# Kernel optimization log

Hardware: AMD Instinct MI355X
Metric: run time of the kernel (lower is better)

Reference implementation:

```python
import jax, jax.numpy as jnp
from jax import lax
import numpy as np

N = 10000      # num_nodes
T = 24         # hist_len
IN_DIM = 16
HID = 128
HEADS = 4
E = 160000     # num_edges
PRED = 24
NEG_SLOPE = 0.2  # GATv2 LeakyReLU default


def _lstm_layer(xs, wih, whh, bih, bhh):
    # xs: [T, N, D]; PyTorch gate order i, f, g, o
    Hh = whh.shape[1]
    h0 = jnp.zeros((xs.shape[1], Hh), xs.dtype)
    def step(carry, xt):
        h, c = carry
        g = xt @ wih.T + bih + h @ whh.T + bhh
        i, f, gg, o = jnp.split(g, 4, axis=-1)
        c = jax.nn.sigmoid(f) * c + jax.nn.sigmoid(i) * jnp.tanh(gg)
        h = jax.nn.sigmoid(o) * jnp.tanh(c)
        return (h, c), h
    (_, _), out = lax.scan(step, (h0, h0), xs)
    return out  # [T, N, Hh]


def _gatv2(z, src, dst, wl, bl, wr, br, att, bias):
    # PyG GATv2Conv: share_weights=False, concat=True, add_self_loops=False
    n = z.shape[0]
    xl = (z @ wl.T + bl).reshape(n, HEADS, HID)   # source/message transform
    xr = (z @ wr.T + br).reshape(n, HEADS, HID)   # target transform
    e = jax.nn.leaky_relu(xl[src] + xr[dst], NEG_SLOPE)   # [E, H, C]
    score = jnp.einsum('ehc,hc->eh', e, att)              # [E, H]
    smax = jax.ops.segment_max(score, dst, num_segments=n)
    p = jnp.exp(score - smax[dst])
    denom = jax.ops.segment_sum(p, dst, num_segments=n)
    alpha = p / (denom[dst] + 1e-16)                      # segment softmax over in-edges
    out = jax.ops.segment_sum(xl[src] * alpha[:, :, None], dst, num_segments=n)
    return out.reshape(n, HEADS * HID) + bias


def setup_inputs() -> dict:
    key = jax.random.key(0)
    ks = iter(jax.random.split(key, 64))
    def W(shape):
        return jax.random.normal(next(ks), shape, jnp.float32) / np.sqrt(shape[-1])
    inp = {}
    inp['x'] = jax.random.normal(next(ks), (N, T, IN_DIM), jnp.float32)
    inp['edge_index'] = jax.random.randint(next(ks), (2, E), 0, N, jnp.int32)
    inp['mlp_in_w0'] = W((HID, IN_DIM)); inp['mlp_in_b0'] = jnp.zeros((HID,), jnp.float32)
    inp['mlp_in_w1'] = W((HID, HID));    inp['mlp_in_b1'] = jnp.zeros((HID,), jnp.float32)
    for l in range(2):  # nn.LSTM(num_layers = lstm_num_layers*2 = 2)
        inp[f'lstm_wih{l}'] = W((4 * HID, HID))
        inp[f'lstm_whh{l}'] = W((4 * HID, HID))
        inp[f'lstm_bih{l}'] = jnp.zeros((4 * HID,), jnp.float32)
        inp[f'lstm_bhh{l}'] = jnp.zeros((4 * HID,), jnp.float32)
    for l in range(2):  # nGAT_layer = 2
        inp[f'gat{l}_wl'] = W((HEADS * HID, HID))
        inp[f'gat{l}_bl'] = jnp.zeros((HEADS * HID,), jnp.float32)
        inp[f'gat{l}_wr'] = W((HEADS * HID, HID))
        inp[f'gat{l}_br'] = jnp.zeros((HEADS * HID,), jnp.float32)
        inp[f'gat{l}_att'] = W((HEADS, HID))
        inp[f'gat{l}_bias'] = jnp.zeros((HEADS * HID,), jnp.float32)
        inp[f'gat{l}_pw'] = W((HID, HEADS * HID))
        inp[f'gat{l}_pb'] = jnp.zeros((HID,), jnp.float32)
    inp['mlp_out_w0'] = W((HID, HID));  inp['mlp_out_b0'] = jnp.zeros((HID,), jnp.float32)
    inp['mlp_out_w1'] = W((PRED, HID)); inp['mlp_out_b1'] = jnp.zeros((PRED,), jnp.float32)
    return inp


def _forward(x, edge_index, mlp_in_w0, mlp_in_b0, mlp_in_w1, mlp_in_b1,
             lstm_wih0, lstm_whh0, lstm_bih0, lstm_bhh0,
             lstm_wih1, lstm_whh1, lstm_bih1, lstm_bhh1,
             gat0_wl, gat0_bl, gat0_wr, gat0_br, gat0_att, gat0_bias, gat0_pw, gat0_pb,
             gat1_wl, gat1_bl, gat1_wr, gat1_br, gat1_att, gat1_bias, gat1_pw, gat1_pb,
             mlp_out_w0, mlp_out_b0, mlp_out_w1, mlp_out_b1):
    src, dst = edge_index[0], edge_index[1]
    h = jnp.transpose(x, (1, 0, 2))                       # [T, N, in_dim]
    # MLP_layers_in: Linear(in,hid), Linear(hid,hid), ReLU
    h = h @ mlp_in_w0.T + mlp_in_b0
    h = jax.nn.relu(h @ mlp_in_w1.T + mlp_in_b1)
    # 2-layer unidirectional LSTM
    h = _lstm_layer(h, lstm_wih0, lstm_whh0, lstm_bih0, lstm_bhh0)
    h = _lstm_layer(h, lstm_wih1, lstm_whh1, lstm_bih1, lstm_bhh1)
    z = h[-1]                                             # [N, HID] last timestep
    # GAT block x2: GATv2Conv -> Linear(heads*hid, hid) -> ReLU
    z = _gatv2(z, src, dst, gat0_wl, gat0_bl, gat0_wr, gat0_br, gat0_att, gat0_bias)
    z = jax.nn.relu(z @ gat0_pw.T + gat0_pb)
    z = _gatv2(z, src, dst, gat1_wl, gat1_bl, gat1_wr, gat1_br, gat1_att, gat1_bias)
    z = jax.nn.relu(z @ gat1_pw.T + gat1_pb)
    # MLP_layers_out: Linear(hid,hid), ReLU, Linear(hid, pred_len)
    z = jax.nn.relu(z @ mlp_out_w0.T + mlp_out_b0)
    return z @ mlp_out_w1.T + mlp_out_b1                  # [N, PRED]


def reference(x, edge_index, mlp_in_w0, mlp_in_b0, mlp_in_w1, mlp_in_b1,
              lstm_wih0, lstm_whh0, lstm_bih0, lstm_bhh0,
              lstm_wih1, lstm_whh1, lstm_bih1, lstm_bhh1,
              gat0_wl, gat0_bl, gat0_wr, gat0_br, gat0_att, gat0_bias, gat0_pw, gat0_pb,
              gat1_wl, gat1_bl, gat1_wr, gat1_br, gat1_att, gat1_bias, gat1_pw, gat1_pb,
              mlp_out_w0, mlp_out_b0, mlp_out_w1, mlp_out_b1):
    return _forward(x, edge_index, mlp_in_w0, mlp_in_b0, mlp_in_w1, mlp_in_b1,
                    lstm_wih0, lstm_whh0, lstm_bih0, lstm_bhh0,
                    lstm_wih1, lstm_whh1, lstm_bih1, lstm_bhh1,
                    gat0_wl, gat0_bl, gat0_wr, gat0_br, gat0_att, gat0_bias, gat0_pw, gat0_pb,
                    gat1_wl, gat1_bl, gat1_wr, gat1_br, gat1_att, gat1_bias, gat1_pw, gat1_pb,
                    mlp_out_w0, mlp_out_b0, mlp_out_w1, mlp_out_b1)
```

## Files before the change

kernel.cpp:

```cpp
#include <hip/hip_runtime.h>
#include <hip/hip_bf16.h>

#define NNODES 10000
#define TLEN 24
#define INDIM 16
#define HID 128
#define GDIM 512

typedef __hip_bfloat16 bf16;
typedef short v8s __attribute__((ext_vector_type(8)));
typedef float v4f __attribute__((ext_vector_type(4)));

__device__ inline float u2f(unsigned u){ return __uint_as_float(u); }

__device__ inline void unpack8(uint4 v, float* f){
  f[0]=u2f(v.x<<16); f[1]=u2f(v.x&0xFFFF0000u);
  f[2]=u2f(v.y<<16); f[3]=u2f(v.y&0xFFFF0000u);
  f[4]=u2f(v.z<<16); f[5]=u2f(v.z&0xFFFF0000u);
  f[6]=u2f(v.w<<16); f[7]=u2f(v.w&0xFFFF0000u);
}

__device__ inline float fsig(float x){
  return __builtin_amdgcn_rcpf(1.f + __expf(-x));
}
__device__ inline float ftanh(float x){
  float t = __expf(-2.f*fabsf(x));
  float r = (1.f - t) * __builtin_amdgcn_rcpf(1.f + t);
  return copysignf(r, x);
}

__global__ __launch_bounds__(256) void conv_w_k(
    const float* s0, const float* s1, const float* s2, const float* s3,
    const float* s4, const float* s5, const float* s6, const float* s7,
    const float* s8, const float* s9, const float* s10,
    bf16* __restrict__ dst, int* __restrict__ deg)
{
  int idx = blockIdx.x*256 + threadIdx.x;
  if (idx < NNODES) deg[idx] = 0;
  if (idx >= 671744) return;
  int c = idx >> 16;
  float v;
  if (c < 10){
    const float* srcs[10] = {s0,s1,s2,s3,s4,s5,s6,s7,s8,s9};
    v = srcs[c][idx & 0xFFFF];
  } else {
    v = s10[idx - 655360];
  }
  dst[idx] = __float2bfloat16(v);
}

__global__ void prep_w_k(
    const float* __restrict__ miw0, const float* __restrict__ mib0,
    const float* __restrict__ miw1, const float* __restrict__ mib1,
    const float* __restrict__ bih0, const float* __restrict__ bhh0,
    const float* __restrict__ bih1, const float* __restrict__ bhh1,
    const float* __restrict__ bl0, const float* __restrict__ br0,
    const float* __restrict__ bl1, const float* __restrict__ br1,
    float* __restrict__ Wp, float* __restrict__ bp,
    float* __restrict__ bsum, float* __restrict__ gblr)
{
  int t = threadIdx.x;
  for (int idx = t; idx < HID*INDIM; idx += 256){
    int j = idx >> 4, d = idx & 15;
    float s = 0.f;
    for (int k=0;k<HID;k++) s += miw1[j*HID+k] * miw0[k*INDIM+d];
    Wp[idx] = s;
  }
  for (int j = t; j < HID; j += 256){
    float s = mib1[j];
    for (int k=0;k<HID;k++) s += miw1[j*HID+k] * mib0[k];
    bp[j] = s;
  }
  for (int i = t; i < GDIM; i += 256){
    bsum[i]        = bih0[i] + bhh0[i];
    bsum[GDIM + i] = bih1[i] + bhh1[i];
  }
  for (int i = t; i < GDIM; i += 256){
    gblr[i]          = bl0[i];
    gblr[GDIM + i]   = br0[i];
    gblr[1024 + i]   = bl1[i];
    gblr[1536 + i]   = br1[i];
  }
}

__global__ __launch_bounds__(256) void mlp_in_k(
    const float* __restrict__ x, const float* __restrict__ Wp,
    const float* __restrict__ bp, bf16* __restrict__ X0)
{
  __shared__ __align__(16) float xs[64*16];
  const int tid = threadIdx.x;
  const int m0 = blockIdx.x*64;
  {
    int row = tid >> 2, q = tid & 3;
    int m = m0 + row;
    int t = m / NNODES, n = m - t*NNODES;
    float4 v = *(const float4*)(x + ((size_t)n*TLEN + t)*INDIM + q*4);
    *(float4*)(xs + row*16 + q*4) = v;
  }
  const int j = tid & 127;
  const int half = tid >> 7;
  const float* wr = Wp + j*INDIM;
  float4 w0 = *(const float4*)(wr);
  float4 w1 = *(const float4*)(wr + 4);
  float4 w2 = *(const float4*)(wr + 8);
  float4 w3 = *(const float4*)(wr + 12);
  float bj = bp[j];
  __syncthreads();
  #pragma unroll 4
  for (int mi=0; mi<32; mi++){
    int row = mi*2 + half;
    const float* xr = xs + row*16;
    float4 a0 = *(const float4*)(xr);
    float4 a1 = *(const float4*)(xr + 4);
    float4 a2 = *(const float4*)(xr + 8);
    float4 a3 = *(const float4*)(xr + 12);
    float s = bj
      + a0.x*w0.x + a0.y*w0.y + a0.z*w0.z + a0.w*w0.w
      + a1.x*w1.x + a1.y*w1.y + a1.z*w1.z + a1.w*w1.w
      + a2.x*w2.x + a2.y*w2.y + a2.z*w2.z + a2.w*w2.w
      + a3.x*w3.x + a3.y*w3.y + a3.z*w3.z + a3.w*w3.w;
    s = s > 0.f ? s : 0.f;
    X0[(size_t)(m0+row)*HID + j] = __float2bfloat16(s);
  }
}

template<int WRITE_ALL>
__global__ __launch_bounds__(512) void lstm_half(
    const bf16* __restrict__ Xin, const bf16* __restrict__ Wih,
    const bf16* __restrict__ Whh, const float* __restrict__ bias,
    bf16* __restrict__ out)
{
  __shared__ __align__(16) bf16 hsA[16*136];
  __shared__ __align__(16) bf16 hsB[16*136];
  const int tid = threadIdx.x;
  const int lane = tid & 63, w = tid >> 6;
  const int r16 = lane & 15, quad = lane >> 4;
  const int m0 = blockIdx.x*16;

  v8s wbi[4][4], wbh[4][4];
  #pragma unroll
  for (int g=0; g<4; g++)
    #pragma unroll
    for (int kc=0; kc<4; kc++){
      size_t o = (size_t)(g*HID + w*16 + r16)*HID + kc*32 + quad*8;
      wbi[g][kc] = *(const v8s*)(Wih + o);
      wbh[g][kc] = *(const v8s*)(Whh + o);
    }
  float bg[4];
  #pragma unroll
  for (int g=0; g<4; g++) bg[g] = bias[g*HID + w*16 + r16];

  const size_t rowoff = (size_t)(m0 + r16) * HID;

  float c[4];
  #pragma unroll
  for (int i=0;i<4;i++) c[i] = 0.f;

  for (int i = tid; i < 272; i += 512){
    *(uint4*)((char*)hsA + i*16) = make_uint4(0,0,0,0);
    *(uint4*)((char*)hsB + i*16) = make_uint4(0,0,0,0);
  }

  v8s ax[4];
  #pragma unroll
  for (int kc=0; kc<4; kc++)
    ax[kc] = *(const v8s*)(Xin + rowoff + kc*32 + quad*8);

  __syncthreads();

  #pragma unroll 1
  for (int t=0; t<TLEN; t++){
    bf16* hrd = (t & 1) ? hsA : hsB;
    bf16* hwr = (t & 1) ? hsB : hsA;

    v4f acc[4];
    #pragma unroll
    for (int g=0;g<4;g++) acc[g] = (v4f)0.f;

    #pragma unroll
    for (int kc=0; kc<4; kc++)
      #pragma unroll
      for (int g=0;g<4;g++)
        acc[g] = __builtin_amdgcn_mfma_f32_16x16x32_bf16(ax[kc], wbi[g][kc], acc[g], 0, 0, 0);

    {
      int tn = t+1 < TLEN ? t+1 : TLEN-1;
      const bf16* Xn = Xin + (size_t)tn*NNODES*HID;
      #pragma unroll
      for (int kc=0; kc<4; kc++)
        ax[kc] = *(const v8s*)(Xn + rowoff + kc*32 + quad*8);
    }

    #pragma unroll
    for (int kc=0; kc<4; kc++){
      v8s av = *(const v8s*)(hrd + r16*136 + kc*32 + quad*8);
      #pragma unroll
      for (int g=0;g<4;g++)
        acc[g] = __builtin_amdgcn_mfma_f32_16x16x32_bf16(av, wbh[g][kc], acc[g], 0, 0, 0);
    }

    #pragma unroll
    for (int r=0;r<4;r++){
      int lrow = quad*4 + r;
      float iv = acc[0][r] + bg[0];
      float fv = acc[1][r] + bg[1];
      float gv = acc[2][r] + bg[2];
      float ov = acc[3][r] + bg[3];
      float ig = fsig(iv), fg = fsig(fv);
      float gg = ftanh(gv), og = fsig(ov);
      float cn = fg*c[r] + ig*gg;
      c[r] = cn;
      hwr[lrow*136 + w*16 + r16] = __float2bfloat16(og*ftanh(cn));
    }
    __syncthreads();

    if (WRITE_ALL){
      bf16* dst = (bf16*)(Xin + (size_t)t*NNODES*HID);
      for (int i = tid; i < 256; i += 512){
        int row = i >> 4, c8 = (i & 15) * 8;
        *(uint4*)(dst + (size_t)(m0+row)*HID + c8) = *(const uint4*)(hwr + row*136 + c8);
      }
    }
  }

  if (!WRITE_ALL){
    const bf16* hfin = ((TLEN-1) & 1) ? hsB : hsA;
    for (int i = tid; i < 256; i += 512){
      int row = i >> 4, c8 = (i & 15) * 8;
      *(uint4*)(out + (size_t)(m0+row)*HID + c8) = *(const uint4*)(hfin + row*136 + c8);
    }
  }
}

template<int ACT>
__global__ __launch_bounds__(256) void gemm_bt(
    const bf16* __restrict__ A, const bf16* __restrict__ B,
    const float* __restrict__ bias, bf16* __restrict__ C,
    int M, int N, int K)
{
  __shared__ __align__(16) bf16 As[128*40];
  __shared__ __align__(16) bf16 Bs[128*40];
  const int tid = threadIdx.x;
  const int m0 = blockIdx.x*128, n0 = blockIdx.y*128;
  const int lane = tid & 63, wave = tid >> 6;
  const int r16 = lane & 15, quad = lane >> 4;

  v4f acc[2][8];
  #pragma unroll
  for (int a=0;a<2;a++)
    #pragma unroll
    for (int b=0;b<8;b++) acc[a][b] = (v4f)0.f;

  for (int k0=0; k0<K; k0+=32){
    #pragma unroll
    for (int i=0;i<2;i++){
      int li = tid + i*256;
      int row = li >> 2, q4 = li & 3;
      uint4 va = make_uint4(0,0,0,0);
      int gm = m0 + row;
      if (gm < M) va = *(const uint4*)(A + (size_t)gm*K + k0 + q4*8);
      *(uint4*)(As + row*40 + q4*8) = va;
      uint4 vb = make_uint4(0,0,0,0);
      int gn = n0 + row;
      if (gn < N) vb = *(const uint4*)(B + (size_t)gn*K + k0 + q4*8);
      *(uint4*)(Bs + row*40 + q4*8) = vb;
    }
    __syncthreads();
    v8s av[2], bv[8];
    #pragma unroll
    for (int mi=0;mi<2;mi++)
      av[mi] = *(const v8s*)(As + (wave*32 + mi*16 + r16)*40 + quad*8);
    #pragma unroll
    for (int ni=0;ni<8;ni++)
      bv[ni] = *(const v8s*)(Bs + (ni*16 + r16)*40 + quad*8);
    #pragma unroll
    for (int mi=0;mi<2;mi++)
      #pragma unroll
      for (int ni=0;ni<8;ni++)
        acc[mi][ni] = __builtin_amdgcn_mfma_f32_16x16x32_bf16(av[mi], bv[ni], acc[mi][ni], 0, 0, 0);
    __syncthreads();
  }

  #pragma unroll
  for (int mi=0;mi<2;mi++){
    #pragma unroll
    for (int r=0;r<4;r++){
      int row = m0 + wave*32 + mi*16 + quad*4 + r;
      if (row >= M) continue;
      #pragma unroll
      for (int ni=0;ni<8;ni++){
        int col = n0 + ni*16 + r16;
        float v = acc[mi][ni][r] + bias[col];
        if (ACT == 1) v = v > 0.f ? v : 0.f;
        C[(size_t)row*N + col] = __float2bfloat16(v);
      }
    }
  }
}

template<int ACT>
__global__ __launch_bounds__(256) void gemm_bt64(
    const bf16* __restrict__ A, const bf16* __restrict__ B,
    const float* __restrict__ bias, bf16* __restrict__ C,
    int M, int K)
{
  __shared__ __align__(16) bf16 As[64*40];
  __shared__ __align__(16) bf16 Bs[128*40];
  const int tid = threadIdx.x;
  const int m0 = blockIdx.x*64;
  const int lane = tid & 63, wave = tid >> 6;
  const int r16 = lane & 15, quad = lane >> 4;

  v4f acc[8];
  #pragma unroll
  for (int b=0;b<8;b++) acc[b] = (v4f)0.f;

  for (int k0=0; k0<K; k0+=32){
    {
      int row = tid >> 2, q4 = tid & 3;
      uint4 va = make_uint4(0,0,0,0);
      int gm = m0 + row;
      if (gm < M) va = *(const uint4*)(A + (size_t)gm*K + k0 + q4*8);
      *(uint4*)(As + row*40 + q4*8) = va;
    }
    #pragma unroll
    for (int i=0;i<2;i++){
      int li = tid + i*256;
      int row = li >> 2, q4 = li & 3;
      uint4 vb = *(const uint4*)(B + (size_t)row*K + k0 + q4*8);
      *(uint4*)(Bs + row*40 + q4*8) = vb;
    }
    __syncthreads();
    v8s av, bv[8];
    av = *(const v8s*)(As + (wave*16 + r16)*40 + quad*8);
    #pragma unroll
    for (int ni=0;ni<8;ni++)
      bv[ni] = *(const v8s*)(Bs + (ni*16 + r16)*40 + quad*8);
    #pragma unroll
    for (int ni=0;ni<8;ni++)
      acc[ni] = __builtin_amdgcn_mfma_f32_16x16x32_bf16(av, bv[ni], acc[ni], 0, 0, 0);
    __syncthreads();
  }

  #pragma unroll
  for (int r=0;r<4;r++){
    int row = m0 + wave*16 + quad*4 + r;
    if (row >= M) continue;
    #pragma unroll
    for (int ni=0;ni<8;ni++){
      int col = ni*16 + r16;
      float v = acc[ni][r] + bias[col];
      if (ACT == 1) v = v > 0.f ? v : 0.f;
      C[(size_t)row*HID + col] = __float2bfloat16(v);
    }
  }
}

__global__ void deg_count_k(const int* __restrict__ dst, int* __restrict__ deg, int E){
  int e = blockIdx.x*256 + threadIdx.x;
  if (e < E){
    unsigned d = (unsigned)dst[e];
    if (d < (unsigned)NNODES) atomicAdd(&deg[d], 1);
  }
}

__global__ void scan_k(const int* __restrict__ deg, int* __restrict__ offs,
                       int* __restrict__ cursor, int n)
{
  __shared__ int part[256];
  __shared__ int base[256];
  int t = threadIdx.x;
  int lo = t*40, hi = lo+40;
  if (lo > n) lo = n;
  if (hi > n) hi = n;
  int s = 0;
  for (int i=lo;i<hi;i++) s += deg[i];
  part[t] = s;
  __syncthreads();
  if (t == 0){
    int run=0;
    for (int i=0;i<256;i++){ base[i]=run; run+=part[i]; }
    offs[n] = run;
  }
  __syncthreads();
  int run = base[t];
  for (int i=lo;i<hi;i++){ offs[i]=run; cursor[i]=run; run += deg[i]; }
}

__global__ void fill_k(const int* __restrict__ src, const int* __restrict__ dst,
                       int* __restrict__ cursor, int* __restrict__ srcs, int E){
  int e = blockIdx.x*256 + threadIdx.x;
  if (e < E){
    unsigned d = (unsigned)dst[e];
    if (d < (unsigned)NNODES){
      int p = atomicAdd(&cursor[d], 1);
      unsigned s = (unsigned)src[e];
      srcs[p] = (s < (unsigned)NNODES) ? (int)s : 0;
    }
  }
}

__global__ __launch_bounds__(256) void gat_onl(
    const int* __restrict__ offs, const int* __restrict__ srcs,
    const bf16* __restrict__ xc, const float* __restrict__ att,
    const float* __restrict__ gbias, bf16* __restrict__ agg)
{
  int d = blockIdx.x*4 + (threadIdx.x >> 6);
  if (d >= NNODES) return;
  int lane = threadIdx.x & 63;
  float fr[8];
  unpack8(*(const uint4*)(xc + (size_t)d*1024 + 512 + lane*8), fr);
  float4 a0 = *(const float4*)(att + lane*8);
  float4 a1 = *(const float4*)(att + lane*8 + 4);
  float fa[8] = {a0.x,a0.y,a0.z,a0.w,a1.x,a1.y,a1.z,a1.w};
  int i0 = offs[d], i1 = offs[d+1];

  float m = -3.4e38f, den = 0.f;
  float acc[8] = {0,0,0,0,0,0,0,0};

  if (i0 < i1){
    uint4 raw = *(const uint4*)(xc + (size_t)srcs[i0]*1024 + lane*8);
    for (int i=i0; i<i1; i++){
      uint4 nxt;
      if (i+1 < i1)
        nxt = *(const uint4*)(xc + (size_t)srcs[i+1]*1024 + lane*8);
      float fl[8];
      unpack8(raw, fl);
      float p = 0.f;
      #pragma unroll
      for (int q=0;q<8;q++){
        float v = fl[q] + fr[q];
        v = v > 0.f ? v : 0.2f*v;
        p += v*fa[q];
      }
      p += __shfl_xor(p, 1); p += __shfl_xor(p, 2);
      p += __shfl_xor(p, 4); p += __shfl_xor(p, 8);
      float mn = fmaxf(m, p);
      float corr = __expf(m - mn);
      float w = __expf(p - mn);
      den = den*corr + w;
      #pragma unroll
      for (int q=0;q<8;q++) acc[q] = acc[q]*corr + w*fl[q];
      m = mn;
      raw = nxt;
    }
  }
  float r = 1.f/(den + 1e-16f);
  float4 b0 = *(const float4*)(gbias + lane*8);
  float4 b1 = *(const float4*)(gbias + lane*8 + 4);
  float fb[8] = {b0.x,b0.y,b0.z,b0.w,b1.x,b1.y,b1.z,b1.w};
  #pragma unroll
  for (int q=0;q<8;q++)
    agg[(size_t)d*GDIM + lane*8 + q] = __float2bfloat16(acc[q]*r + fb[q]);
}

__global__ __launch_bounds__(256) void mlp_final_k(
    const bf16* __restrict__ a, const float* __restrict__ w,
    const float* __restrict__ b, float* __restrict__ out)
{
  int g = blockIdx.x*256 + threadIdx.x;
  if (g >= NNODES*24) return;
  int j = g % 24;
  int row = g / 24;
  const bf16* ar = a + (size_t)row*HID;
  const float* wr = w + (size_t)j*HID;
  float s = b[j];
  for (int k=0;k<HID;k+=8){
    float fa[8];
    unpack8(*(const uint4*)(ar+k), fa);
    float4 w0 = *(const float4*)(wr + k);
    float4 w1 = *(const float4*)(wr + k + 4);
    s += fa[0]*w0.x + fa[1]*w0.y + fa[2]*w0.z + fa[3]*w0.w
       + fa[4]*w1.x + fa[5]*w1.y + fa[6]*w1.z + fa[7]*w1.w;
  }
  out[g] = s;
}


extern "C" void kernel_launch(void* const* d_in, const int* in_sizes, int n_in,
                              void* d_out, int out_size, void* d_ws, size_t ws_size,
                              hipStream_t stream)
{
  const float* x   = (const float*)d_in[0];
  const int*   ei  = (const int*)d_in[1];
  const int E = in_sizes[1] / 2;
  const int* srcp = ei;
  const int* dstp = ei + E;

  const float* miw0 = (const float*)d_in[2];
  const float* mib0 = (const float*)d_in[3];
  const float* miw1 = (const float*)d_in[4];
  const float* mib1 = (const float*)d_in[5];
  const float* wih0 = (const float*)d_in[6];
  const float* whh0 = (const float*)d_in[7];
  const float* bih0 = (const float*)d_in[8];
  const float* bhh0 = (const float*)d_in[9];
  const float* wih1 = (const float*)d_in[10];
  const float* whh1 = (const float*)d_in[11];
  const float* bih1 = (const float*)d_in[12];
  const float* bhh1 = (const float*)d_in[13];
  const float* g_wl[2]   = {(const float*)d_in[14], (const float*)d_in[22]};
  const float* g_bl[2]   = {(const float*)d_in[15], (const float*)d_in[23]};
  const float* g_wr[2]   = {(const float*)d_in[16], (const float*)d_in[24]};
  const float* g_br[2]   = {(const float*)d_in[17], (const float*)d_in[25]};
  const float* g_att[2]  = {(const float*)d_in[18], (const float*)d_in[26]};
  const float* g_bias[2] = {(const float*)d_in[19], (const float*)d_in[27]};
  const float* g_pw[2]   = {(const float*)d_in[20], (const float*)d_in[28]};
  const float* g_pb[2]   = {(const float*)d_in[21], (const float*)d_in[29]};
  const float* mow0 = (const float*)d_in[30];
  const float* mob0 = (const float*)d_in[31];
  const float* mow1 = (const float*)d_in[32];
  const float* mob1 = (const float*)d_in[33];
  (void)n_in; (void)out_size; (void)ws_size;

  char* base = (char*)d_ws;
  size_t off = 0;
  auto carve = [&](size_t n)->char*{
    char* p = base + off;
    off = (off + n + 255) & ~(size_t)255;
    return p;
  };
  char*  X0r = carve((size_t)TLEN*NNODES*HID*2);
  bf16*  zf  = (bf16*)carve((size_t)NNODES*HID*2);
  float* Wp  = (float*)carve(HID*INDIM*4);
  float* bp  = (float*)carve(HID*4);
  float* bsum= (float*)carve(2*GDIM*4);
  float* gblr= (float*)carve(2*1024*4);
  bf16*  wbf = (bf16*)carve((size_t)671744*2);
  int*   offsb = (int*)carve((size_t)(NNODES+1)*4);
  int*   curs  = (int*)carve((size_t)NNODES*4);
  int*   srcs  = (int*)carve((size_t)E*4);
  int*   deg   = (int*)carve((size_t)NNODES*4);
  bf16*  agg   = (bf16*)carve((size_t)NNODES*GDIM*2);

  const bf16* wih0b = wbf + 0;
  const bf16* whh0b = wbf + 65536;
  const bf16* wih1b = wbf + 131072;
  const bf16* whh1b = wbf + 196608;
  const bf16* wlr0b = wbf + 262144;
  const bf16* pw0b  = wbf + 393216;
  const bf16* wlr1b = wbf + 458752;
  const bf16* pw1b  = wbf + 589824;
  const bf16* mow0b = wbf + 655360;
  const bf16* wlrb[2] = {wlr0b, wlr1b};
  const bf16* pwb[2]  = {pw0b, pw1b};

  bf16* X0 = (bf16*)X0r;
  bf16* xc = (bf16*)X0r;
  bf16* z2 = (bf16*)(X0r + 20480000);
  bf16* z3 = (bf16*)(X0r + 23040000);
  bf16* o0 = (bf16*)(X0r + 25600000);

  conv_w_k<<<2624, 256, 0, stream>>>(wih0, whh0, wih1, whh1,
                                     g_wl[0], g_wr[0], g_pw[0],
                                     g_wl[1], g_wr[1], g_pw[1], mow0, wbf, deg);
  prep_w_k<<<1, 256, 0, stream>>>(miw0, mib0, miw1, mib1,
                                  bih0, bhh0, bih1, bhh1,
                                  g_bl[0], g_br[0], g_bl[1], g_br[1],
                                  Wp, bp, bsum, gblr);

  mlp_in_k<<<(TLEN*NNODES)/64, 256, 0, stream>>>(x, Wp, bp, X0);

  deg_count_k<<<(E+255)/256, 256, 0, stream>>>(dstp, deg, E);
  scan_k<<<1, 256, 0, stream>>>(deg, offsb, curs, NNODES);
  fill_k<<<(E+255)/256, 256, 0, stream>>>(srcp, dstp, curs, srcs, E);

  const int NBL = NNODES / 16;
  lstm_half<1><<<NBL, 512, 0, stream>>>(X0, wih0b, whh0b, bsum, nullptr);
  lstm_half<0><<<NBL, 512, 0, stream>>>(X0, wih1b, whh1b, bsum + GDIM, zf);

  const bf16* zin = zf;
  bf16* zouts[2] = {z2, z3};
  const int NB64 = (NNODES + 63) / 64;
  for (int l=0; l<2; l++){
    gemm_bt<0><<<dim3(79,8), 256, 0, stream>>>(zin, wlrb[l], gblr + l*1024, xc, NNODES, 1024, HID);
    gat_onl<<<(NNODES+3)/4, 256, 0, stream>>>(offsb, srcs, xc, g_att[l], g_bias[l], agg);
    gemm_bt64<1><<<NB64, 256, 0, stream>>>(agg, pwb[l], g_pb[l], zouts[l], NNODES, GDIM);
    zin = zouts[l];
  }

  gemm_bt64<1><<<NB64, 256, 0, stream>>>(z3, mow0b, mob0, o0, NNODES, HID);
  mlp_final_k<<<(NNODES*24+255)/256, 256, 0, stream>>>(o0, mow1, mob1, (float*)d_out);
}
```

Before: 606.0 us.

## Fuse output MLP layers, deepen GAT gather prefetch, parallelize weight prep

Fuses the final two output MLP layers into one kernel, so the intermediate hidden activations stay in shared memory instead of making a round trip through global memory, and one launch is removed. The GAT aggregation loop now prefetches two neighbor rows ahead instead of one, to hide more gather latency at the cost of extra registers. The single-block prep_w_k weight precompute is split across 9 blocks. These are three independent small changes.

```diff
diff --git a/kernel.cpp b/kernel.cpp
--- a/kernel.cpp
+++ b/kernel.cpp
@@ -49,7 +49,7 @@
   dst[idx] = __float2bfloat16(v);
 }
 
-__global__ void prep_w_k(
+__global__ __launch_bounds__(256) void prep_w_k(
     const float* __restrict__ miw0, const float* __restrict__ mib0,
     const float* __restrict__ miw1, const float* __restrict__ mib1,
     const float* __restrict__ bih0, const float* __restrict__ bhh0,
@@ -60,16 +60,19 @@
     float* __restrict__ bsum, float* __restrict__ gblr)
 {
   int t = threadIdx.x;
-  for (int idx = t; idx < HID*INDIM; idx += 256){
+  int b = blockIdx.x;
+  if (b < 8){
+    int idx = b*256 + t;
     int j = idx >> 4, d = idx & 15;
     float s = 0.f;
     for (int k=0;k<HID;k++) s += miw1[j*HID+k] * miw0[k*INDIM+d];
     Wp[idx] = s;
-  }
-  for (int j = t; j < HID; j += 256){
-    float s = mib1[j];
-    for (int k=0;k<HID;k++) s += miw1[j*HID+k] * mib0[k];
-    bp[j] = s;
+    return;
+  }
+  if (t < HID){
+    float s = mib1[t];
+    for (int k=0;k<HID;k++) s += miw1[t*HID+k] * mib0[k];
+    bp[t] = s;
   }
   for (int i = t; i < GDIM; i += 256){
     bsum[i]        = bih0[i] + bhh0[i];
@@ -356,6 +359,81 @@
   }
 }
 
+__global__ __launch_bounds__(256) void mlp_out_fused_k(
+    const bf16* __restrict__ A, const bf16* __restrict__ B,
+    const float* __restrict__ bias, const float* __restrict__ w1,
+    const float* __restrict__ b1, float* __restrict__ out, int M)
+{
+  __shared__ __align__(16) bf16 As[64*40];
+  __shared__ __align__(16) bf16 Bs[128*40];
+  __shared__ __align__(16) bf16 o0s[64*136];
+  const int tid = threadIdx.x;
+  const int m0 = blockIdx.x*64;
+  const int lane = tid & 63, wave = tid >> 6;
+  const int r16 = lane & 15, quad = lane >> 4;
+
+  v4f acc[8];
+  #pragma unroll
+  for (int b=0;b<8;b++) acc[b] = (v4f)0.f;
+
+  for (int k0=0; k0<HID; k0+=32){
+    {
+      int row = tid >> 2, q4 = tid & 3;
+      uint4 va = make_uint4(0,0,0,0);
+      int gm = m0 + row;
+      if (gm < M) va = *(const uint4*)(A + (size_t)gm*HID + k0 + q4*8);
+      *(uint4*)(As + row*40 + q4*8) = va;
+    }
+    #pragma unroll
+    for (int i=0;i<2;i++){
+      int li = tid + i*256;
+      int row = li >> 2, q4 = li & 3;
+      uint4 vb = *(const uint4*)(B + (size_t)row*HID + k0 + q4*8);
+      *(uint4*)(Bs + row*40 + q4*8) = vb;
+    }
+    __syncthreads();
+    v8s av, bv[8];
+    av = *(const v8s*)(As + (wave*16 + r16)*40 + quad*8);
+    #pragma unroll
+    for (int ni=0;ni<8;ni++)
+      bv[ni] = *(const v8s*)(Bs + (ni*16 + r16)*40 + quad*8);
+    #pragma unroll
+    for (int ni=0;ni<8;ni++)
+      acc[ni] = __builtin_amdgcn_mfma_f32_16x16x32_bf16(av, bv[ni], acc[ni], 0, 0, 0);
+    __syncthreads();
+  }
+
+  #pragma unroll
+  for (int r=0;r<4;r++){
+    int row = wave*16 + quad*4 + r;
+    #pragma unroll
+    for (int ni=0;ni<8;ni++){
+      int col = ni*16 + r16;
+      float v = acc[ni][r] + bias[col];
+      v = v > 0.f ? v : 0.f;
+      o0s[row*136 + col] = __float2bfloat16(v);
+    }
+  }
+  __syncthreads();
+
+  for (int idx = tid; idx < 64*24; idx += 256){
+    int row = idx / 24, j = idx - row*24;
+    if (m0 + row >= M) continue;
+    const bf16* ar = o0s + row*136;
+    const float* wr = w1 + j*HID;
+    float s = b1[j];
+    for (int k=0;k<HID;k+=8){
+      float fa[8];
+      unpack8(*(const uint4*)(ar+k), fa);
+      float4 w0 = *(const float4*)(wr + k);
+      float4 w1v = *(const float4*)(wr + k + 4);
+      s += fa[0]*w0.x + fa[1]*w0.y + fa[2]*w0.z + fa[3]*w0.w
+         + fa[4]*w1v.x + fa[5]*w1v.y + fa[6]*w1v.z + fa[7]*w1v.w;
+    }
+    out[(size_t)(m0+row)*24 + j] = s;
+  }
+}
+
 __global__ void deg_count_k(const int* __restrict__ dst, int* __restrict__ deg, int E){
   int e = blockIdx.x*256 + threadIdx.x;
   if (e < E){
@@ -419,13 +497,14 @@
   float acc[8] = {0,0,0,0,0,0,0,0};
 
   if (i0 < i1){
-    uint4 raw = *(const uint4*)(xc + (size_t)srcs[i0]*1024 + lane*8);
+    uint4 r0 = *(const uint4*)(xc + (size_t)srcs[i0]*1024 + lane*8);
+    uint4 r1 = r0;
+    if (i0+1 < i1) r1 = *(const uint4*)(xc + (size_t)srcs[i0+1]*1024 + lane*8);
     for (int i=i0; i<i1; i++){
-      uint4 nxt;
-      if (i+1 < i1)
-        nxt = *(const uint4*)(xc + (size_t)srcs[i+1]*1024 + lane*8);
+      uint4 r2 = r1;
+      if (i+2 < i1) r2 = *(const uint4*)(xc + (size_t)srcs[i+2]*1024 + lane*8);
       float fl[8];
-      unpack8(raw, fl);
+      unpack8(r0, fl);
       float p = 0.f;
       #pragma unroll
       for (int q=0;q<8;q++){
@@ -442,7 +521,7 @@
       #pragma unroll
       for (int q=0;q<8;q++) acc[q] = acc[q]*corr + w*fl[q];
       m = mn;
-      raw = nxt;
+      r0 = r1; r1 = r2;
     }
   }
   float r = 1.f/(den + 1e-16f);
@@ -452,28 +531,6 @@
   #pragma unroll
   for (int q=0;q<8;q++)
     agg[(size_t)d*GDIM + lane*8 + q] = __float2bfloat16(acc[q]*r + fb[q]);
-}
-
-__global__ __launch_bounds__(256) void mlp_final_k(
-    const bf16* __restrict__ a, const float* __restrict__ w,
-    const float* __restrict__ b, float* __restrict__ out)
-{
-  int g = blockIdx.x*256 + threadIdx.x;
-  if (g >= NNODES*24) return;
-  int j = g % 24;
-  int row = g / 24;
-  const bf16* ar = a + (size_t)row*HID;
-  const float* wr = w + (size_t)j*HID;
-  float s = b[j];
-  for (int k=0;k<HID;k+=8){
-    float fa[8];
-    unpack8(*(const uint4*)(ar+k), fa);
-    float4 w0 = *(const float4*)(wr + k);
-    float4 w1 = *(const float4*)(wr + k + 4);
-    s += fa[0]*w0.x + fa[1]*w0.y + fa[2]*w0.z + fa[3]*w0.w
-       + fa[4]*w1.x + fa[5]*w1.y + fa[6]*w1.z + fa[7]*w1.w;
-  }
-  out[g] = s;
 }
 
 
@@ -549,12 +606,11 @@
   bf16* xc = (bf16*)X0r;
   bf16* z2 = (bf16*)(X0r + 20480000);
   bf16* z3 = (bf16*)(X0r + 23040000);
-  bf16* o0 = (bf16*)(X0r + 25600000);
 
   conv_w_k<<<2624, 256, 0, stream>>>(wih0, whh0, wih1, whh1,
                                      g_wl[0], g_wr[0], g_pw[0],
                                      g_wl[1], g_wr[1], g_pw[1], mow0, wbf, deg);
-  prep_w_k<<<1, 256, 0, stream>>>(miw0, mib0, miw1, mib1,
+  prep_w_k<<<9, 256, 0, stream>>>(miw0, mib0, miw1, mib1,
                                   bih0, bhh0, bih1, bhh1,
                                   g_bl[0], g_br[0], g_bl[1], g_br[1],
                                   Wp, bp, bsum, gblr);
@@ -579,6 +635,6 @@
     zin = zouts[l];
   }
 
-  gemm_bt64<1><<<NB64, 256, 0, stream>>>(z3, mow0b, mob0, o0, NNODES, HID);
-  mlp_final_k<<<(NNODES*24+255)/256, 256, 0, stream>>>(o0, mow1, mob1, (float*)d_out);
-}
+  mlp_out_fused_k<<<NB64, 256, 0, stream>>>(z3, mow0b, mob0, mow1, mob1,
+                                            (float*)d_out, NNODES);
+}
```

Result: faster. 578.0 us (-4.6%).
